# Performance work log

Measured on AMD Instinct MI355X. Metric: run time of the kernel, lower is better.

## Reference

```python
import jax, jax.numpy as jnp
import numpy as np

N_NODES = 50000
N_EDGES = 500000
D_MODEL = 128
NHEAD = 8
D_HEAD = 16
NUM_KEYS = 8
NUM_ETYPES = 4
NUM_STRINGS = 20000
NUM_BLOCKS = 2
N_TARGETS = 128


def setup_inputs() -> dict:
    key = jax.random.key(0)
    ks = jax.random.split(key, 16)
    s = 1.0 / np.sqrt(D_MODEL)
    return {
        "emb": jax.random.normal(ks[0], (NUM_STRINGS, D_MODEL), jnp.float32) * s,
        "query_w": jax.random.normal(ks[1], (NUM_BLOCKS, NUM_KEYS, NHEAD, D_HEAD, D_MODEL), jnp.float32) * s,
        "key_w": jax.random.normal(ks[2], (NUM_BLOCKS, NUM_ETYPES, NHEAD, D_HEAD, D_MODEL), jnp.float32) * s,
        "value_w": jax.random.normal(ks[3], (NUM_BLOCKS, NUM_ETYPES, NHEAD, D_HEAD, D_MODEL), jnp.float32) * s,
        "node_w": jax.random.normal(ks[4], (NUM_BLOCKS, NUM_KEYS, NHEAD, D_HEAD, D_MODEL), jnp.float32) * s,
        "target_w": jax.random.normal(ks[5], (NUM_BLOCKS, NUM_KEYS, NHEAD, D_HEAD), jnp.float32) * s,
        "ln_gamma": jnp.ones((NUM_BLOCKS, D_MODEL), jnp.float32),
        "ln_beta": jnp.zeros((NUM_BLOCKS, D_MODEL), jnp.float32),
        "value_ids": jax.random.randint(ks[6], (N_NODES,), 0, NUM_STRINGS),
        "key_ids": jax.random.randint(ks[7], (N_NODES,), 0, NUM_KEYS),
        "src": jax.random.randint(ks[8], (N_EDGES,), 0, N_NODES),
        "dst": jax.random.randint(ks[9], (N_EDGES,), 0, N_NODES),
        "etype": jax.random.randint(ks[10], (N_EDGES,), 0, NUM_ETYPES),
        "target_idx": jax.random.randint(ks[11], (N_TARGETS,), 0, N_NODES),
    }


def _layer_norm(x, g, b, eps=1e-5):
    mu = jnp.mean(x, -1, keepdims=True)
    var = jnp.var(x, -1, keepdims=True)
    return (x - mu) * jax.lax.rsqrt(var + eps) * g + b


def _per_type_proj(feat, w, type_ids):
    # feat: [N,D], w: [T,H,Dh,D] -> project for all types then select the
    # node's/edge-endpoint's own type (identical math to gathering w[type]).
    all_t = jnp.einsum("nd,thfd->nthf", feat, w)  # [N,T,H,Dh]
    return jnp.take_along_axis(all_t, type_ids[:, None, None, None], axis=1)[:, 0]


def _hetero_attn_conv(feat, qw, kw, vw, nw, lg, lb, key_ids, src, dst, etype):
    n = feat.shape[0]
    q = _per_type_proj(feat, qw, key_ids)                     # [N,H,Dh] per-key query
    k_all = jnp.einsum("nd,thfd->nthf", feat, kw)             # [N,T,H,Dh]
    v_all = jnp.einsum("nd,thfd->nthf", feat, vw)
    k_e = k_all[src, etype]                                   # [E,H,Dh] per-etype key
    v_e = v_all[src, etype]                                   # [E,H,Dh]
    scale = np.float32(1.0 / np.sqrt(D_HEAD))
    scores = jnp.sum(q[dst] * k_e, -1) * scale                # [E,H]
    # edge softmax over incoming edges of each dst node
    m = jax.ops.segment_max(scores, dst, num_segments=n)      # [N,H]
    e = jnp.exp(scores - m[dst])
    z = jax.ops.segment_sum(e, dst, num_segments=n)
    attn = e / (z[dst] + 1e-9)                                # [E,H]
    agg = jax.ops.segment_sum(attn[..., None] * v_e, dst, num_segments=n)
    agg = agg.reshape(n, D_MODEL)
    h = _per_type_proj(agg, nw, key_ids).reshape(n, D_MODEL)  # per-key node proj
    h = jax.nn.relu(h)                                        # node_activation='relu'
    return _layer_norm(h, lg, lb)                             # norm=True


def reference(emb, query_w, key_w, value_w, node_w, target_w, ln_gamma, ln_beta,
              value_ids, key_ids, src, dst, etype, target_idx):
    feat = emb[value_ids]  # ValueEmbedding lookup [N,D]
    target_keys = key_ids[target_idx]
    outs = []
    for i in range(NUM_BLOCKS):
        prev = feat
        feat = _hetero_attn_conv(feat, query_w[i], key_w[i], value_w[i], node_w[i],
                                 ln_gamma[i], ln_beta[i], key_ids, src, dst, etype)
        feat = feat + prev  # block_residual=True (conv_residual=False)
        tf = feat[target_idx].reshape(N_TARGETS, NHEAD, D_HEAD)
        tw = target_w[i][target_keys]  # [B,H,Dh]
        outs.append(jnp.sum(tf * tw, axis=(1, 2)))  # Target readout per block
    out = jnp.mean(jnp.stack(outs, -1), -1)  # mean over block outputs
    return out  # [N_TARGETS] (single target)
```

## Files before the change

kernel.cpp:

```cpp
#include <hip/hip_runtime.h>
#include <hip/hip_bf16.h>

#define N_NODES   50000
#define N_EDGES   500000
#define NHEAD     8
#define NUM_KEYS  8
#define NUM_ETYPES 4
#define NUM_BLOCKS 2
#define N_TARGETS 128
#define NPAD      51200
#define NTILES    400
#define NBLK      196
#define LDWF      132
#define SCAP      45

typedef unsigned short u16;
typedef unsigned int   u32;
typedef __attribute__((ext_vector_type(8))) short short8;
typedef __attribute__((ext_vector_type(4))) short short4v;
typedef __attribute__((ext_vector_type(4))) float floatx4;

__device__ __forceinline__ size_t pkaddr(int tile, int r, int c){
  return (size_t)tile * 16384 + ((c >> 3) << 10) + (r << 3) + (c & 7);
}

__device__ __forceinline__ float bflo(u32 u)  { return __uint_as_float(u << 16); }
__device__ __forceinline__ float bfhi(u32 u)  { return __uint_as_float(u & 0xffff0000u); }
__device__ __forceinline__ float bf2f(u16 u)  { return __uint_as_float(((u32)u) << 16); }
__device__ __forceinline__ u16   f2bf(float f){
  u32 u = __float_as_uint(f);
  u += 0x7fffu + ((u >> 16) & 1u);
  return (u16)(u >> 16);
}

__global__ void detect_dtype(const u16* raw, int* flag){
  __shared__ int cnt;
  if (threadIdx.x == 0) cnt = 0;
  __syncthreads();
  int sane = 0;
  #pragma unroll
  for (int k = 0; k < 4; k++){
    u16 u = raw[threadIdx.x * 4 + k];
    int e = (u >> 7) & 0xff;
    if (e >= 100 && e <= 145) sane++;
  }
  atomicAdd(&cnt, sane);
  __syncthreads();
  if (threadIdx.x == 0) *flag = (cnt >= 870) ? 1 : 0;
}

__global__ void pack_all(const void* qw, const void* nw, const void* kw, const void* vw,
                         const void* tw, const void* lg, const void* lb,
                         u16* qwc, u16* nwc, u16* kvw, float* twf, float* gbf,
                         const int* __restrict__ flag){
  int i = blockIdx.x * 256 + threadIdx.x;
  int F = *flag;
  if (i < 786432){
    int tile = i >> 14, rem = i & 16383;
    int row = rem >> 7, col = rem & 127;
    const void* src; int sidx; u16* dst; int dtile;
    if (tile < 16){ src = qw; sidx = i; dst = qwc; dtile = tile; }
    else if (tile < 32){ src = nw; sidx = i - 262144; dst = nwc; dtile = tile - 16; }
    else if (tile < 40){ int t = tile - 32; src = kw; sidx = i - 524288;
      dst = kvw; dtile = (t >> 2) * 8 + (t & 3); }
    else { int t = tile - 40; src = vw; sidx = i - 655360;
      dst = kvw; dtile = (t >> 2) * 8 + 4 + (t & 3); }
    u16 v = F ? ((const u16*)src)[sidx] : f2bf(((const float*)src)[sidx]);
    dst[pkaddr(dtile, row, col)] = v;
  } else if (i < 788992){
    int j = i - 786432;
    if (j < 2048)      twf[j] = F ? bf2f(((const u16*)tw)[j]) : ((const float*)tw)[j];
    else if (j < 2304){ int k = j - 2048; gbf[k]       = F ? bf2f(((const u16*)lg)[k]) : ((const float*)lg)[k]; }
    else              { int k = j - 2304; gbf[256 + k] = F ? bf2f(((const u16*)lb)[k]) : ((const float*)lb)[k]; }
  }
}

__global__ void khist_blk(const int* __restrict__ key_ids, int* __restrict__ blkcnt){
  __shared__ int c[8];
  int t = threadIdx.x, b = blockIdx.x;
  if (t < 8) c[t] = 0;
  __syncthreads();
  int n = b * 256 + t;
  if (n < N_NODES) atomicAdd(&c[key_ids[n]], 1);
  __syncthreads();
  if (t < 8) blkcnt[t * NBLK + b] = c[t];
}
__global__ void kscan2(const int* __restrict__ blkcnt, int* __restrict__ base,
                       int* __restrict__ tile_key){
  __shared__ int po[8];
  __shared__ int tot[8];
  int t = threadIdx.x;
  if (t < 8){
    int s = 0;
    for (int b = 0; b < NBLK; b++) s += blkcnt[t * NBLK + b];
    tot[t] = s;
  }
  __syncthreads();
  if (t == 0){
    int off = 0;
    for (int k = 0; k < 8; k++){ po[k] = off; off += ((tot[k] + 127) >> 7) << 7; }
  }
  __syncthreads();
  if (t < 8){
    int run = po[t];
    for (int b = 0; b < NBLK; b++){ base[t * NBLK + b] = run; run += blkcnt[t * NBLK + b]; }
  }
  for (int tt = t; tt < NTILES; tt += 64){
    int row = tt << 7, k = 7;
    for (int kk = 1; kk < 8; kk++)
      if (row < po[kk]){ k = kk - 1; break; }
    tile_key[tt] = k;
  }
}
__global__ void scatter_perm2(const int* __restrict__ key_ids, const int* __restrict__ base,
                              int* __restrict__ perm, int* __restrict__ invperm){
  __shared__ unsigned char keyarr[256];
  int t = threadIdx.x, b = blockIdx.x;
  int n = b * 256 + t;
  int key = (n < N_NODES) ? key_ids[n] : 8;
  keyarr[t] = (unsigned char)key;
  __syncthreads();
  if (n >= N_NODES) return;
  int rank = 0;
  for (int j = 0; j < t; j++) rank += (keyarr[j] == (unsigned char)key);
  int pos = base[key * NBLK + b] + rank;
  perm[pos] = n;
  invperm[n] = pos;
}

__global__ void gather_feat(const void* emb_raw, const int* __restrict__ vid,
                            const int* __restrict__ perm, const int* __restrict__ flag,
                            float* __restrict__ feat, u16* __restrict__ fhi,
                            u16* __restrict__ flo){
  int i = blockIdx.x * 256 + threadIdx.x;
  int n = i >> 7, d = i & 127;
  int e = (vid[perm[n]] << 7) + d;
  float v = (*flag) ? bf2f(((const u16*)emb_raw)[e]) : ((const float*)emb_raw)[e];
  feat[i] = v;
  u16 h = f2bf(v);
  size_t pa = pkaddr(n >> 7, n & 127, d);
  fhi[pa] = h;
  flo[pa] = f2bf(v - bf2f(h));
}

__global__ void hist_dst(const int* __restrict__ dst, const int* __restrict__ invp,
                         int* __restrict__ deg){
  int e = blockIdx.x * 256 + threadIdx.x;
  if (e < N_EDGES) atomicAdd(&deg[invp[dst[e]]], 1);
}
__global__ __launch_bounds__(1024) void scan_deg(const int* __restrict__ deg,
                                                 int* __restrict__ rs, int* __restrict__ cur){
  __shared__ int s[1024];
  int t = threadIdx.x;
  int lo = t * 50, hi = lo + 50;
  int sum = 0;
  for (int i = lo; i < hi; i++) sum += deg[i];
  s[t] = sum;
  __syncthreads();
  for (int off = 1; off < 1024; off <<= 1){
    int v = (t >= off) ? s[t - off] : 0;
    __syncthreads();
    s[t] += v;
    __syncthreads();
  }
  int run = s[t] - sum;
  for (int i = lo; i < hi; i++){
    rs[i] = run; cur[i] = run;
    run += deg[i];
  }
}
__global__ void scatter_edges(const int* __restrict__ src, const int* __restrict__ dst,
                              const int* __restrict__ et, const int* __restrict__ invp,
                              int* __restrict__ cur, u32* __restrict__ epk){
  int e = blockIdx.x * 256 + threadIdx.x;
  if (e >= N_EDGES) return;
  int pos = atomicAdd(&cur[invp[dst[e]]], 1);
  epk[pos] = ((u32)invp[src[e]] << 2) | (u32)et[e];
}
__global__ __launch_bounds__(256) void sort_csr(const int* __restrict__ rs,
                                                const int* __restrict__ deg,
                                                u32* __restrict__ epk){
  __shared__ u32 buf[256 * SCAP];
  int t = threadIdx.x;
  int n = blockIdx.x * 256 + t;
  if (n >= NPAD) return;
  int s = rs[n], c = deg[n];
  if (c <= 1) return;
  if (c <= SCAP){
    u32* b = buf + t * SCAP;
    for (int i = 0; i < c; i++) b[i] = epk[s + i];
    for (int i = 1; i < c; i++){
      u32 v = b[i];
      int j = i - 1;
      while (j >= 0 && b[j] > v){ b[j + 1] = b[j]; j--; }
      b[j + 1] = v;
    }
    for (int i = 0; i < c; i++) epk[s + i] = b[i];
  } else {
    for (int i = 1; i < c; i++){
      u32 v = epk[s + i];
      int j = i - 1;
      while (j >= 0 && epk[s + j] > v){ epk[s + j + 1] = epk[s + j]; j--; }
      epk[s + j + 1] = v;
    }
  }
}

__global__ __launch_bounds__(256) void gemm_qkv(
    const u16* __restrict__ Ahi, const u16* __restrict__ Alo,
    const u16* __restrict__ Qw, const u16* __restrict__ KVw,
    const int* __restrict__ tkey,
    float* __restrict__ qf32, float* __restrict__ kf32, u16* __restrict__ vbf)
{
  int id = blockIdx.x;
  int xcd = id & 7, wi = id >> 3;
  int cy = xcd * 50 + wi / 9;
  int cx = wi % 9;
  const u16* Bte = (cx == 0) ? (Qw + (size_t)tkey[cy] * 16384)
                             : (KVw + (size_t)(cx - 1) * 16384);
  const u16* Ath = Ahi + (size_t)cy * 16384;
  const u16* Atl = Alo + (size_t)cy * 16384;
  int w = threadIdx.x >> 6, l = threadIdx.x & 63;
  int wm = (w & 1) * 64, wn = (w >> 1) * 64;
  int lr = l & 15, lgp = l >> 4;
  floatx4 acc[4][4] = {};
  #pragma unroll
  for (int kk = 0; kk < 4; kk++){
    int cc10 = (kk * 4 + lgp) << 10;
    short8 ah[4], al[4], bfr[4];
    #pragma unroll
    for (int i = 0; i < 4; i++){
      int off = cc10 + ((wm + i * 16 + lr) << 3);
      ah[i] = *(const short8*)(Ath + off);
      al[i] = *(const short8*)(Atl + off);
    }
    #pragma unroll
    for (int j = 0; j < 4; j++)
      bfr[j] = *(const short8*)(Bte + cc10 + ((wn + j * 16 + lr) << 3));
    #pragma unroll
    for (int i = 0; i < 4; i++)
      #pragma unroll
      for (int j = 0; j < 4; j++){
        acc[i][j] = __builtin_amdgcn_mfma_f32_16x16x32_bf16(ah[i], bfr[j], acc[i][j], 0, 0, 0);
        acc[i][j] = __builtin_amdgcn_mfma_f32_16x16x32_bf16(al[i], bfr[j], acc[i][j], 0, 0, 0);
      }
  }
  int rbase = (cy << 7) + wm + (lgp << 2);
  int cbase = wn + lr;
  if (cx == 0){
    #pragma unroll
    for (int i = 0; i < 4; i++)
      #pragma unroll
      for (int r = 0; r < 4; r++){
        size_t ro = (size_t)(rbase + i * 16 + r) << 7;
        #pragma unroll
        for (int j = 0; j < 4; j++)
          qf32[ro + cbase + j * 16] = acc[i][j][r];
      }
  } else if (cx <= 4){
    int et = cx - 1;
    #pragma unroll
    for (int i = 0; i < 4; i++)
      #pragma unroll
      for (int r = 0; r < 4; r++){
        size_t ro = ((size_t)((rbase + i * 16 + r) << 2) + et) << 7;
        #pragma unroll
        for (int j = 0; j < 4; j++)
          kf32[ro + cbase + j * 16] = acc[i][j][r];
      }
  } else {
    int et = cx - 5;
    #pragma unroll
    for (int i = 0; i < 4; i++)
      #pragma unroll
      for (int r = 0; r < 4; r++){
        size_t ro = ((size_t)((rbase + i * 16 + r) << 2) + et) << 7;
        #pragma unroll
        for (int j = 0; j < 4; j++)
          vbf[ro + cbase + j * 16] = f2bf(acc[i][j][r]);
      }
  }
}

__global__ __launch_bounds__(256) void gemm_h_ln(
    const u16* __restrict__ Ahi, const u16* __restrict__ Alo,
    const u16* __restrict__ Bt, const int* __restrict__ tkey,
    const float* __restrict__ gbf,
    float* __restrict__ feat, u16* __restrict__ fhi, u16* __restrict__ flo, int blk)
{
  __shared__ float scf[64 * LDWF];
  int m0 = blockIdx.x * 64;
  int tile = blockIdx.x >> 1, rbase = (blockIdx.x & 1) * 64;
  const u16* Bte = Bt + (size_t)tkey[tile] * 16384;
  const u16* Ath = Ahi + (size_t)tile * 16384;
  const u16* Atl = Alo + (size_t)tile * 16384;
  int w = threadIdx.x >> 6, l = threadIdx.x & 63;
  int wn = w * 32;
  int lr = l & 15, lgp = l >> 4;
  floatx4 acc[4][2] = {};
  #pragma unroll
  for (int kk = 0; kk < 4; kk++){
    int cc10 = (kk * 4 + lgp) << 10;
    short8 ah[4], al[4], bfr[2];
    #pragma unroll
    for (int i = 0; i < 4; i++){
      int off = cc10 + ((rbase + i * 16 + lr) << 3);
      ah[i] = *(const short8*)(Ath + off);
      al[i] = *(const short8*)(Atl + off);
    }
    #pragma unroll
    for (int j = 0; j < 2; j++)
      bfr[j] = *(const short8*)(Bte + cc10 + ((wn + j * 16 + lr) << 3));
    #pragma unroll
    for (int i = 0; i < 4; i++)
      #pragma unroll
      for (int j = 0; j < 2; j++){
        acc[i][j] = __builtin_amdgcn_mfma_f32_16x16x32_bf16(ah[i], bfr[j], acc[i][j], 0, 0, 0);
        acc[i][j] = __builtin_amdgcn_mfma_f32_16x16x32_bf16(al[i], bfr[j], acc[i][j], 0, 0, 0);
      }
  }
  #pragma unroll
  for (int i = 0; i < 4; i++)
    #pragma unroll
    for (int j = 0; j < 2; j++)
      #pragma unroll
      for (int r = 0; r < 4; r++)
        scf[(i * 16 + lgp * 4 + r) * LDWF + wn + j * 16 + lr] = acc[i][j][r];
  __syncthreads();
  int r = threadIdx.x >> 2, q4 = (threadIdx.x & 3) * 32;
  const float* srow = scf + r * LDWF + q4;
  float s1 = 0.f, s2 = 0.f;
  #pragma unroll
  for (int c = 0; c < 32; c++){
    float v = fmaxf(srow[c], 0.f);
    s1 += v; s2 += v * v;
  }
  s1 += __shfl_xor(s1, 1, 64); s1 += __shfl_xor(s1, 2, 64);
  s2 += __shfl_xor(s2, 1, 64); s2 += __shfl_xor(s2, 2, 64);
  float mu = s1 * (1.f / 128.f);
  float var = s2 * (1.f / 128.f) - mu * mu;
  float rstd = rsqrtf(var + 1e-5f);
  int n = m0 + r;
  int ntile = n >> 7, nr = n & 127;
  float* fr = feat + (size_t)n * 128 + q4;
  const float* gp = gbf + (blk << 7) + q4;
  #pragma unroll
  for (int c = 0; c < 32; c += 4){
    float4 fo = *(float4*)(fr + c);
    float y0 = (fmaxf(srow[c+0], 0.f) - mu) * rstd * gp[c+0] + gp[256 + c + 0] + fo.x;
    float y1 = (fmaxf(srow[c+1], 0.f) - mu) * rstd * gp[c+1] + gp[256 + c + 1] + fo.y;
    float y2 = (fmaxf(srow[c+2], 0.f) - mu) * rstd * gp[c+2] + gp[256 + c + 2] + fo.z;
    float y3 = (fmaxf(srow[c+3], 0.f) - mu) * rstd * gp[c+3] + gp[256 + c + 3] + fo.w;
    *(float4*)(fr + c) = make_float4(y0, y1, y2, y3);
    u16 h0 = f2bf(y0), h1 = f2bf(y1), h2 = f2bf(y2), h3 = f2bf(y3);
    size_t pa = pkaddr(ntile, nr, q4 + c);
    short4v ph; ph.x = (short)h0; ph.y = (short)h1; ph.z = (short)h2; ph.w = (short)h3;
    *(short4v*)(fhi + pa) = ph;
    short4v pl;
    pl.x = (short)f2bf(y0 - bf2f(h0)); pl.y = (short)f2bf(y1 - bf2f(h1));
    pl.z = (short)f2bf(y2 - bf2f(h2)); pl.w = (short)f2bf(y3 - bf2f(h3));
    *(short4v*)(flo + pa) = pl;
  }
}

__device__ __forceinline__ void edge_body(const float* kp, const u16* vp,
                                          const float* qf, float& z, float* acc){
  float4 k0 = *(const float4*)kp,       k1 = *(const float4*)(kp + 4);
  float4 k2 = *(const float4*)(kp + 8), k3 = *(const float4*)(kp + 12);
  uint4 v0 = *(const uint4*)vp, v1 = *(const uint4*)(vp + 8);
  float s = 0.f;
  s = fmaf(qf[0],  k0.x, s); s = fmaf(qf[1],  k0.y, s);
  s = fmaf(qf[2],  k0.z, s); s = fmaf(qf[3],  k0.w, s);
  s = fmaf(qf[4],  k1.x, s); s = fmaf(qf[5],  k1.y, s);
  s = fmaf(qf[6],  k1.z, s); s = fmaf(qf[7],  k1.w, s);
  s = fmaf(qf[8],  k2.x, s); s = fmaf(qf[9],  k2.y, s);
  s = fmaf(qf[10], k2.z, s); s = fmaf(qf[11], k2.w, s);
  s = fmaf(qf[12], k3.x, s); s = fmaf(qf[13], k3.y, s);
  s = fmaf(qf[14], k3.z, s); s = fmaf(qf[15], k3.w, s);
  float ew = __expf(fminf(s * 0.25f, 80.f));
  z += ew;
  acc[0]  += ew * bflo(v0.x); acc[1]  += ew * bfhi(v0.x);
  acc[2]  += ew * bflo(v0.y); acc[3]  += ew * bfhi(v0.y);
  acc[4]  += ew * bflo(v0.z); acc[5]  += ew * bfhi(v0.z);
  acc[6]  += ew * bflo(v0.w); acc[7]  += ew * bfhi(v0.w);
  acc[8]  += ew * bflo(v1.x); acc[9]  += ew * bfhi(v1.x);
  acc[10] += ew * bflo(v1.y); acc[11] += ew * bfhi(v1.y);
  acc[12] += ew * bflo(v1.z); acc[13] += ew * bfhi(v1.z);
  acc[14] += ew * bflo(v1.w); acc[15] += ew * bfhi(v1.w);
}

__global__ __launch_bounds__(256) void edge_attn(
    const float* __restrict__ qf32, const float* __restrict__ kf32,
    const u16* __restrict__ vbf,
    const int* __restrict__ rs, const int* __restrict__ deg,
    const u32* __restrict__ epk, u16* __restrict__ agghi, u16* __restrict__ agglo)
{
  int n = blockIdx.x * 4 + (threadIdx.x >> 6);
  int l = threadIdx.x & 63;
  int h = l & 7, s = l >> 3;
  int c0 = h << 4;
  const float* qp = qf32 + ((size_t)n << 7) + c0;
  float qf[16];
  #pragma unroll
  for (int d = 0; d < 16; d += 4){
    float4 qv = *(const float4*)(qp + d);
    qf[d] = qv.x; qf[d+1] = qv.y; qf[d+2] = qv.z; qf[d+3] = qv.w;
  }
  int e0 = rs[n], cnt = deg[n];
  float z = 0.f;
  float acc[16];
  #pragma unroll
  for (int j = 0; j < 16; j++) acc[j] = 0.f;
  for (int base = 0; base < cnt; base += 16){
    int idx0 = base + s, idx1 = base + s + 8;
    bool p0 = idx0 < cnt, p1 = idx1 < cnt;
    u32 pk0 = p0 ? epk[e0 + idx0] : 0u;
    u32 pk1 = p1 ? epk[e0 + idx1] : 0u;
    size_t t0 = ((size_t)((pk0 >> 2) << 2) + (pk0 & 3)) << 7;
    size_t t1 = ((size_t)((pk1 >> 2) << 2) + (pk1 & 3)) << 7;
    if (p0) edge_body(kf32 + t0 + c0, vbf + t0 + c0, qf, z, acc);
    if (p1) edge_body(kf32 + t1 + c0, vbf + t1 + c0, qf, z, acc);
  }
  #pragma unroll
  for (int m = 8; m < 64; m <<= 1){
    z += __shfl_xor(z, m, 64);
    #pragma unroll
    for (int j = 0; j < 16; j++) acc[j] += __shfl_xor(acc[j], m, 64);
  }
  float inv = 1.f / (z + 1e-9f);
  int j0 = s * 2;
  float x0 = acc[j0] * inv, x1 = acc[j0 + 1] * inv;
  u16 h0 = f2bf(x0), h1 = f2bf(x1);
  int col = (h << 4) + j0;
  size_t pa = pkaddr(n >> 7, n & 127, col);
  *(u32*)(agghi + pa) = (u32)h0 | ((u32)h1 << 16);
  *(u32*)(agglo + pa) = (u32)f2bf(x0 - bf2f(h0)) | ((u32)f2bf(x1 - bf2f(h1)) << 16);
}

__global__ __launch_bounds__(128) void readout(
    const float* __restrict__ feat, const float* __restrict__ twf,
    const int* __restrict__ key_ids, const int* __restrict__ invp,
    const int* __restrict__ tgt,
    float* __restrict__ outacc, void* dout, const int* __restrict__ flag, int blk)
{
  int t = threadIdx.x;
  int n = tgt[t];
  int key = key_ids[n];
  const float* fr = feat + (size_t)invp[n] * 128;
  const float* wr = twf + (size_t)((blk * 8 + key) << 7);
  float acc = 0.f;
  #pragma unroll
  for (int d = 0; d < 128; d++) acc = fmaf(fr[d], wr[d], acc);
  if (blk == 0){
    outacc[t] = 0.5f * acc;
  } else {
    float r = outacc[t] + 0.5f * acc;
    if (*flag) ((u16*)dout)[t] = f2bf(r);
    else       ((float*)dout)[t] = r;
  }
}

extern "C" void kernel_launch(void* const* d_in, const int* in_sizes, int n_in,
                              void* d_out, int out_size, void* d_ws, size_t ws_size,
                              hipStream_t stream)
{
  const void* emb = d_in[0];
  const void* qw  = d_in[1];
  const void* kw  = d_in[2];
  const void* vw  = d_in[3];
  const void* nw  = d_in[4];
  const void* tw  = d_in[5];
  const void* lg  = d_in[6];
  const void* lb  = d_in[7];
  const int* value_ids = (const int*)d_in[8];
  const int* key_ids   = (const int*)d_in[9];
  const int* srcp  = (const int*)d_in[10];
  const int* dstp  = (const int*)d_in[11];
  const int* etp   = (const int*)d_in[12];
  const int* tgt   = (const int*)d_in[13];

  char* p = (char*)d_ws;
  auto carve = [&](size_t bytes)->char*{
    char* r = p; p += (bytes + 255) & ~(size_t)255; return r;
  };
  int*   flag    = (int*)  carve(4);
  float* featp   = (float*)carve((size_t)NPAD * 128 * 4);
  u16*   feathi  = (u16*)  carve((size_t)NPAD * 128 * 2);
  u16*   featlo  = (u16*)  carve((size_t)NPAD * 128 * 2);
  u16*   qwc     = (u16*)  carve((size_t)2 * 1024 * 128 * 2);
  u16*   kvw     = (u16*)  carve((size_t)2 * 1024 * 128 * 2);
  u16*   nwc     = (u16*)  carve((size_t)2 * 1024 * 128 * 2);
  float* twf     = (float*)carve((size_t)2048 * 4);
  float* gbf     = (float*)carve((size_t)512 * 4);
  int*   blkcnt  = (int*)  carve((size_t)8 * NBLK * 4);
  int*   kbase   = (int*)  carve((size_t)8 * NBLK * 4);
  int*   tile_key= (int*)  carve(NTILES * 4);
  int*   perm    = (int*)  carve((size_t)NPAD * 4);
  int*   invperm = (int*)  carve((size_t)N_NODES * 4);
  int*   deg     = (int*)  carve((size_t)NPAD * 4);
  int*   rsx     = (int*)  carve((size_t)NPAD * 4);
  int*   cur     = (int*)  carve((size_t)NPAD * 4);
  u32*   epk     = (u32*)  carve((size_t)N_EDGES * 4);
  float* qf32    = (float*)carve((size_t)NPAD * 128 * 4);
  float* kf32    = (float*)carve((size_t)NPAD * 512 * 4);
  u16*   vbf     = (u16*)  carve((size_t)NPAD * 512 * 2);
  u16*   agghi   = (u16*)  carve((size_t)NPAD * 128 * 2);
  u16*   agglo   = (u16*)  carve((size_t)NPAD * 128 * 2);
  float* outacc  = (float*)carve((size_t)N_TARGETS * 4);
  (void)ws_size; (void)n_in; (void)in_sizes; (void)out_size;

  detect_dtype<<<1, 256, 0, stream>>>((const u16*)emb, flag);

  pack_all<<<3083, 256, 0, stream>>>(qw, nw, kw, vw, tw, lg, lb,
                                     qwc, nwc, kvw, twf, gbf, flag);

  hipMemsetAsync(perm, 0, (size_t)NPAD * 4, stream);
  khist_blk<<<NBLK, 256, 0, stream>>>(key_ids, blkcnt);
  kscan2<<<1, 64, 0, stream>>>(blkcnt, kbase, tile_key);
  scatter_perm2<<<NBLK, 256, 0, stream>>>(key_ids, kbase, perm, invperm);

  gather_feat<<<(NPAD * 128) / 256, 256, 0, stream>>>(emb, value_ids, perm, flag,
                                                      featp, feathi, featlo);

  hipMemsetAsync(deg, 0, (size_t)NPAD * 4, stream);
  const int eg = (N_EDGES + 255) / 256;
  hist_dst<<<eg, 256, 0, stream>>>(dstp, invperm, deg);
  scan_deg<<<1, 1024, 0, stream>>>(deg, rsx, cur);
  scatter_edges<<<eg, 256, 0, stream>>>(srcp, dstp, etp, invperm, cur, epk);
  sort_csr<<<(NPAD + 255) / 256, 256, 0, stream>>>(rsx, deg, epk);

  for (int b = 0; b < NUM_BLOCKS; b++){
    gemm_qkv<<<3600, 256, 0, stream>>>(feathi, featlo,
                                       qwc + (size_t)b * 1024 * 128,
                                       kvw + (size_t)b * 1024 * 128,
                                       tile_key, qf32, kf32, vbf);
    edge_attn<<<NPAD / 4, 256, 0, stream>>>(qf32, kf32, vbf, rsx, deg, epk, agghi, agglo);
    gemm_h_ln<<<NPAD / 64, 256, 0, stream>>>(agghi, agglo,
                                             nwc + (size_t)b * 1024 * 128,
                                             tile_key, gbf, featp, feathi, featlo, b);
    readout<<<1, 128, 0, stream>>>(featp, twf, key_ids, invperm, tgt, outacc, d_out, flag, b);
  }
}
```

Before: 554.5 us.

## Merge setup kernels and compute LayerNorm stats from registers in gemm_h_ln

```diff
diff --git a/kernel.cpp b/kernel.cpp
--- a/kernel.cpp
+++ b/kernel.cpp
@@ -11,7 +11,6 @@
 #define NPAD      51200
 #define NTILES    400
 #define NBLK      196
-#define LDWF      132
 #define SCAP      45
 
 typedef unsigned short u16;
@@ -33,85 +32,89 @@
   return (u16)(u >> 16);
 }
 
-__global__ void detect_dtype(const u16* raw, int* flag){
-  __shared__ int cnt;
-  if (threadIdx.x == 0) cnt = 0;
-  __syncthreads();
-  int sane = 0;
-  #pragma unroll
-  for (int k = 0; k < 4; k++){
-    u16 u = raw[threadIdx.x * 4 + k];
-    int e = (u >> 7) & 0xff;
-    if (e >= 100 && e <= 145) sane++;
-  }
-  atomicAdd(&cnt, sane);
-  __syncthreads();
-  if (threadIdx.x == 0) *flag = (cnt >= 870) ? 1 : 0;
-}
-
-__global__ void pack_all(const void* qw, const void* nw, const void* kw, const void* vw,
-                         const void* tw, const void* lg, const void* lb,
-                         u16* qwc, u16* nwc, u16* kvw, float* twf, float* gbf,
-                         const int* __restrict__ flag){
-  int i = blockIdx.x * 256 + threadIdx.x;
-  int F = *flag;
-  if (i < 786432){
-    int tile = i >> 14, rem = i & 16383;
-    int row = rem >> 7, col = rem & 127;
-    const void* src; int sidx; u16* dst; int dtile;
-    if (tile < 16){ src = qw; sidx = i; dst = qwc; dtile = tile; }
-    else if (tile < 32){ src = nw; sidx = i - 262144; dst = nwc; dtile = tile - 16; }
-    else if (tile < 40){ int t = tile - 32; src = kw; sidx = i - 524288;
-      dst = kvw; dtile = (t >> 2) * 8 + (t & 3); }
-    else { int t = tile - 40; src = vw; sidx = i - 655360;
-      dst = kvw; dtile = (t >> 2) * 8 + 4 + (t & 3); }
-    u16 v = F ? ((const u16*)src)[sidx] : f2bf(((const float*)src)[sidx]);
-    dst[pkaddr(dtile, row, col)] = v;
-  } else if (i < 788992){
-    int j = i - 786432;
-    if (j < 2048)      twf[j] = F ? bf2f(((const u16*)tw)[j]) : ((const float*)tw)[j];
-    else if (j < 2304){ int k = j - 2048; gbf[k]       = F ? bf2f(((const u16*)lg)[k]) : ((const float*)lg)[k]; }
-    else              { int k = j - 2304; gbf[256 + k] = F ? bf2f(((const u16*)lb)[k]) : ((const float*)lb)[k]; }
-  }
-}
-
-__global__ void khist_blk(const int* __restrict__ key_ids, int* __restrict__ blkcnt){
-  __shared__ int c[8];
-  int t = threadIdx.x, b = blockIdx.x;
-  if (t < 8) c[t] = 0;
-  __syncthreads();
-  int n = b * 256 + t;
-  if (n < N_NODES) atomicAdd(&c[key_ids[n]], 1);
-  __syncthreads();
-  if (t < 8) blkcnt[t * NBLK + b] = c[t];
-}
-__global__ void kscan2(const int* __restrict__ blkcnt, int* __restrict__ base,
-                       int* __restrict__ tile_key){
-  __shared__ int po[8];
-  __shared__ int tot[8];
-  int t = threadIdx.x;
-  if (t < 8){
-    int s = 0;
-    for (int b = 0; b < NBLK; b++) s += blkcnt[t * NBLK + b];
-    tot[t] = s;
-  }
-  __syncthreads();
-  if (t == 0){
-    int off = 0;
-    for (int k = 0; k < 8; k++){ po[k] = off; off += ((tot[k] + 127) >> 7) << 7; }
-  }
-  __syncthreads();
-  if (t < 8){
-    int run = po[t];
-    for (int b = 0; b < NBLK; b++){ base[t * NBLK + b] = run; run += blkcnt[t * NBLK + b]; }
-  }
-  for (int tt = t; tt < NTILES; tt += 64){
-    int row = tt << 7, k = 7;
-    for (int kk = 1; kk < 8; kk++)
-      if (row < po[kk]){ k = kk - 1; break; }
-    tile_key[tt] = k;
-  }
-}
+__global__ void k_detect_khist(const u16* raw, int* flag,
+                               const int* __restrict__ key_ids, int* __restrict__ blkcnt){
+  if (blockIdx.x == 0){
+    __shared__ int cnt;
+    if (threadIdx.x == 0) cnt = 0;
+    __syncthreads();
+    int sane = 0;
+    #pragma unroll
+    for (int k = 0; k < 4; k++){
+      u16 u = raw[threadIdx.x * 4 + k];
+      int e = (u >> 7) & 0xff;
+      if (e >= 100 && e <= 145) sane++;
+    }
+    atomicAdd(&cnt, sane);
+    __syncthreads();
+    if (threadIdx.x == 0) *flag = (cnt >= 870) ? 1 : 0;
+  } else {
+    __shared__ int c[8];
+    int t = threadIdx.x, b = blockIdx.x - 1;
+    if (t < 8) c[t] = 0;
+    __syncthreads();
+    int n = b * 256 + t;
+    if (n < N_NODES) atomicAdd(&c[key_ids[n]], 1);
+    __syncthreads();
+    if (t < 8) blkcnt[t * NBLK + b] = c[t];
+  }
+}
+
+__global__ void k_pack_kscan(const void* qw, const void* nw, const void* kw, const void* vw,
+                             const void* tw, const void* lg, const void* lb,
+                             u16* qwc, u16* nwc, u16* kvw, float* twf, float* gbf,
+                             const int* __restrict__ flag,
+                             const int* __restrict__ blkcnt, int* __restrict__ base,
+                             int* __restrict__ tile_key){
+  if (blockIdx.x < 3082){
+    int i = blockIdx.x * 256 + threadIdx.x;
+    int F = *flag;
+    if (i < 786432){
+      int tile = i >> 14, rem = i & 16383;
+      int row = rem >> 7, col = rem & 127;
+      const void* src; int sidx; u16* dst; int dtile;
+      if (tile < 16){ src = qw; sidx = i; dst = qwc; dtile = tile; }
+      else if (tile < 32){ src = nw; sidx = i - 262144; dst = nwc; dtile = tile - 16; }
+      else if (tile < 40){ int t = tile - 32; src = kw; sidx = i - 524288;
+        dst = kvw; dtile = (t >> 2) * 8 + (t & 3); }
+      else { int t = tile - 40; src = vw; sidx = i - 655360;
+        dst = kvw; dtile = (t >> 2) * 8 + 4 + (t & 3); }
+      u16 v = F ? ((const u16*)src)[sidx] : f2bf(((const float*)src)[sidx]);
+      dst[pkaddr(dtile, row, col)] = v;
+    } else if (i < 788992){
+      int j = i - 786432;
+      if (j < 2048)      twf[j] = F ? bf2f(((const u16*)tw)[j]) : ((const float*)tw)[j];
+      else if (j < 2304){ int k = j - 2048; gbf[k]       = F ? bf2f(((const u16*)lg)[k]) : ((const float*)lg)[k]; }
+      else              { int k = j - 2304; gbf[256 + k] = F ? bf2f(((const u16*)lb)[k]) : ((const float*)lb)[k]; }
+    }
+  } else {
+    __shared__ int po[8];
+    __shared__ int tot[8];
+    int t = threadIdx.x;
+    if (t < 8){
+      int s = 0;
+      for (int b = 0; b < NBLK; b++) s += blkcnt[t * NBLK + b];
+      tot[t] = s;
+    }
+    __syncthreads();
+    if (t == 0){
+      int off = 0;
+      for (int k = 0; k < 8; k++){ po[k] = off; off += ((tot[k] + 127) >> 7) << 7; }
+    }
+    __syncthreads();
+    if (t < 8){
+      int run = po[t];
+      for (int b = 0; b < NBLK; b++){ base[t * NBLK + b] = run; run += blkcnt[t * NBLK + b]; }
+    }
+    for (int tt = t; tt < NTILES; tt += 256){
+      int row = tt << 7, k = 7;
+      for (int kk = 1; kk < 8; kk++)
+        if (row < po[kk]){ k = kk - 1; break; }
+      tile_key[tt] = k;
+    }
+  }
+}
+
 __global__ void scatter_perm2(const int* __restrict__ key_ids, const int* __restrict__ base,
                               int* __restrict__ perm, int* __restrict__ invperm){
   __shared__ unsigned char keyarr[256];
@@ -128,26 +131,28 @@
   invperm[n] = pos;
 }
 
-__global__ void gather_feat(const void* emb_raw, const int* __restrict__ vid,
-                            const int* __restrict__ perm, const int* __restrict__ flag,
-                            float* __restrict__ feat, u16* __restrict__ fhi,
-                            u16* __restrict__ flo){
-  int i = blockIdx.x * 256 + threadIdx.x;
-  int n = i >> 7, d = i & 127;
-  int e = (vid[perm[n]] << 7) + d;
-  float v = (*flag) ? bf2f(((const u16*)emb_raw)[e]) : ((const float*)emb_raw)[e];
-  feat[i] = v;
-  u16 h = f2bf(v);
-  size_t pa = pkaddr(n >> 7, n & 127, d);
-  fhi[pa] = h;
-  flo[pa] = f2bf(v - bf2f(h));
-}
-
-__global__ void hist_dst(const int* __restrict__ dst, const int* __restrict__ invp,
-                         int* __restrict__ deg){
-  int e = blockIdx.x * 256 + threadIdx.x;
-  if (e < N_EDGES) atomicAdd(&deg[invp[dst[e]]], 1);
-}
+__global__ void k_gather_hist(const void* emb_raw, const int* __restrict__ vid,
+                              const int* __restrict__ perm, const int* __restrict__ flag,
+                              float* __restrict__ feat, u16* __restrict__ fhi,
+                              u16* __restrict__ flo,
+                              const int* __restrict__ dst, const int* __restrict__ invp,
+                              int* __restrict__ deg){
+  if (blockIdx.x < 25600){
+    int i = blockIdx.x * 256 + threadIdx.x;
+    int n = i >> 7, d = i & 127;
+    int e = (vid[perm[n]] << 7) + d;
+    float v = (*flag) ? bf2f(((const u16*)emb_raw)[e]) : ((const float*)emb_raw)[e];
+    feat[i] = v;
+    u16 h = f2bf(v);
+    size_t pa = pkaddr(n >> 7, n & 127, d);
+    fhi[pa] = h;
+    flo[pa] = f2bf(v - bf2f(h));
+  } else {
+    int e = (blockIdx.x - 25600) * 256 + threadIdx.x;
+    if (e < N_EDGES) atomicAdd(&deg[invp[dst[e]]], 1);
+  }
+}
+
 __global__ __launch_bounds__(1024) void scan_deg(const int* __restrict__ deg,
                                                  int* __restrict__ rs, int* __restrict__ cur){
   __shared__ int s[1024];
@@ -288,7 +293,7 @@
     const float* __restrict__ gbf,
     float* __restrict__ feat, u16* __restrict__ fhi, u16* __restrict__ flo, int blk)
 {
-  __shared__ float scf[64 * LDWF];
+  __shared__ float part[64][8];
   int m0 = blockIdx.x * 64;
   int tile = blockIdx.x >> 1, rbase = (blockIdx.x & 1) * 64;
   const u16* Bte = Bt + (size_t)tkey[tile] * 16384;
@@ -320,46 +325,51 @@
       }
   }
   #pragma unroll
-  for (int i = 0; i < 4; i++)
-    #pragma unroll
-    for (int j = 0; j < 2; j++)
-      #pragma unroll
-      for (int r = 0; r < 4; r++)
-        scf[(i * 16 + lgp * 4 + r) * LDWF + wn + j * 16 + lr] = acc[i][j][r];
+  for (int i = 0; i < 4; i++){
+    #pragma unroll
+    for (int r = 0; r < 4; r++){
+      float v0 = fmaxf(acc[i][0][r], 0.f);
+      float v1 = fmaxf(acc[i][1][r], 0.f);
+      float s1 = v0 + v1;
+      float s2 = v0 * v0 + v1 * v1;
+      #pragma unroll
+      for (int m = 1; m < 16; m <<= 1){
+        s1 += __shfl_xor(s1, m, 64);
+        s2 += __shfl_xor(s2, m, 64);
+      }
+      if (lr == 0){
+        int row = i * 16 + lgp * 4 + r;
+        part[row][w * 2]     = s1;
+        part[row][w * 2 + 1] = s2;
+      }
+    }
+  }
   __syncthreads();
-  int r = threadIdx.x >> 2, q4 = (threadIdx.x & 3) * 32;
-  const float* srow = scf + r * LDWF + q4;
-  float s1 = 0.f, s2 = 0.f;
-  #pragma unroll
-  for (int c = 0; c < 32; c++){
-    float v = fmaxf(srow[c], 0.f);
-    s1 += v; s2 += v * v;
-  }
-  s1 += __shfl_xor(s1, 1, 64); s1 += __shfl_xor(s1, 2, 64);
-  s2 += __shfl_xor(s2, 1, 64); s2 += __shfl_xor(s2, 2, 64);
-  float mu = s1 * (1.f / 128.f);
-  float var = s2 * (1.f / 128.f) - mu * mu;
-  float rstd = rsqrtf(var + 1e-5f);
-  int n = m0 + r;
-  int ntile = n >> 7, nr = n & 127;
-  float* fr = feat + (size_t)n * 128 + q4;
-  const float* gp = gbf + (blk << 7) + q4;
-  #pragma unroll
-  for (int c = 0; c < 32; c += 4){
-    float4 fo = *(float4*)(fr + c);
-    float y0 = (fmaxf(srow[c+0], 0.f) - mu) * rstd * gp[c+0] + gp[256 + c + 0] + fo.x;
-    float y1 = (fmaxf(srow[c+1], 0.f) - mu) * rstd * gp[c+1] + gp[256 + c + 1] + fo.y;
-    float y2 = (fmaxf(srow[c+2], 0.f) - mu) * rstd * gp[c+2] + gp[256 + c + 2] + fo.z;
-    float y3 = (fmaxf(srow[c+3], 0.f) - mu) * rstd * gp[c+3] + gp[256 + c + 3] + fo.w;
-    *(float4*)(fr + c) = make_float4(y0, y1, y2, y3);
-    u16 h0 = f2bf(y0), h1 = f2bf(y1), h2 = f2bf(y2), h3 = f2bf(y3);
-    size_t pa = pkaddr(ntile, nr, q4 + c);
-    short4v ph; ph.x = (short)h0; ph.y = (short)h1; ph.z = (short)h2; ph.w = (short)h3;
-    *(short4v*)(fhi + pa) = ph;
-    short4v pl;
-    pl.x = (short)f2bf(y0 - bf2f(h0)); pl.y = (short)f2bf(y1 - bf2f(h1));
-    pl.z = (short)f2bf(y2 - bf2f(h2)); pl.w = (short)f2bf(y3 - bf2f(h3));
-    *(short4v*)(flo + pa) = pl;
+  const float* gp = gbf + (blk << 7);
+  #pragma unroll
+  for (int i = 0; i < 4; i++){
+    #pragma unroll
+    for (int r = 0; r < 4; r++){
+      int row = i * 16 + lgp * 4 + r;
+      float s1 = part[row][0] + part[row][2] + part[row][4] + part[row][6];
+      float s2 = part[row][1] + part[row][3] + part[row][5] + part[row][7];
+      float mu = s1 * (1.f / 128.f);
+      float var = s2 * (1.f / 128.f) - mu * mu;
+      float rstd = rsqrtf(var + 1e-5f);
+      int n = m0 + row;
+      int ntile = n >> 7, nr = n & 127;
+      #pragma unroll
+      for (int j = 0; j < 2; j++){
+        int col = wn + j * 16 + lr;
+        float y = (fmaxf(acc[i][j][r], 0.f) - mu) * rstd * gp[col] + gp[256 + col]
+                + feat[((size_t)n << 7) + col];
+        feat[((size_t)n << 7) + col] = y;
+        u16 h = f2bf(y);
+        size_t pa = pkaddr(ntile, nr, col);
+        fhi[pa] = h;
+        flo[pa] = f2bf(y - bf2f(h));
+      }
+    }
   }
 }
 
@@ -496,8 +506,8 @@
   int*   kbase   = (int*)  carve((size_t)8 * NBLK * 4);
   int*   tile_key= (int*)  carve(NTILES * 4);
   int*   perm    = (int*)  carve((size_t)NPAD * 4);
+  int*   deg     = (int*)  carve((size_t)NPAD * 4);
   int*   invperm = (int*)  carve((size_t)N_NODES * 4);
-  int*   deg     = (int*)  carve((size_t)NPAD * 4);
   int*   rsx     = (int*)  carve((size_t)NPAD * 4);
   int*   cur     = (int*)  carve((size_t)NPAD * 4);
   u32*   epk     = (u32*)  carve((size_t)N_EDGES * 4);
@@ -509,24 +519,16 @@
   float* outacc  = (float*)carve((size_t)N_TARGETS * 4);
   (void)ws_size; (void)n_in; (void)in_sizes; (void)out_size;
 
-  detect_dtype<<<1, 256, 0, stream>>>((const u16*)emb, flag);
-
-  pack_all<<<3083, 256, 0, stream>>>(qw, nw, kw, vw, tw, lg, lb,
-                                     qwc, nwc, kvw, twf, gbf, flag);
-
-  hipMemsetAsync(perm, 0, (size_t)NPAD * 4, stream);
-  khist_blk<<<NBLK, 256, 0, stream>>>(key_ids, blkcnt);
-  kscan2<<<1, 64, 0, stream>>>(blkcnt, kbase, tile_key);
+  hipMemsetAsync(perm, 0, (size_t)2 * NPAD * 4, stream);
+  k_detect_khist<<<NBLK + 1, 256, 0, stream>>>((const u16*)emb, flag, key_ids, blkcnt);
+  k_pack_kscan<<<3083, 256, 0, stream>>>(qw, nw, kw, vw, tw, lg, lb,
+                                         qwc, nwc, kvw, twf, gbf, flag,
+                                         blkcnt, kbase, tile_key);
   scatter_perm2<<<NBLK, 256, 0, stream>>>(key_ids, kbase, perm, invperm);
-
-  gather_feat<<<(NPAD * 128) / 256, 256, 0, stream>>>(emb, value_ids, perm, flag,
-                                                      featp, feathi, featlo);
-
-  hipMemsetAsync(deg, 0, (size_t)NPAD * 4, stream);
-  const int eg = (N_EDGES + 255) / 256;
-  hist_dst<<<eg, 256, 0, stream>>>(dstp, invperm, deg);
+  k_gather_hist<<<25600 + (N_EDGES + 255) / 256, 256, 0, stream>>>(
+      emb, value_ids, perm, flag, featp, feathi, featlo, dstp, invperm, deg);
   scan_deg<<<1, 1024, 0, stream>>>(deg, rsx, cur);
-  scatter_edges<<<eg, 256, 0, stream>>>(srcp, dstp, etp, invperm, cur, epk);
+  scatter_edges<<<(N_EDGES + 255) / 256, 256, 0, stream>>>(srcp, dstp, etp, invperm, cur, epk);
   sort_csr<<<(NPAD + 255) / 256, 256, 0, stream>>>(rsx, deg, epk);
 
   for (int b = 0; b < NUM_BLOCKS; b++){
```

After: 535.8 us. 1.03x faster.
